# Kernel tuning notes

Hardware: AMD Instinct MI355X
Metric: run time of the kernel (lower is better)

Reference implementation:

```python
import jax, jax.numpy as jnp
import numpy as np

# ---- config ----
N = 500000
C = 32            # output_coordinate_dim
RES = [256, 256, 256, 64]
J = 2             # wavelet levels
BOUNDS = 1.3
# plane i -> (H, W) of stored plane, and (q, r) coord indices into [x,y,z,t]
# grid_sample convention: coord0 indexes W, coord1 indexes H
PLANE_RES = [(256, 256), (256, 256), (256, 64), (256, 256), (256, 64), (256, 64)]
COORD_IDX = [(0, 1), (0, 2), (3, 0), (1, 2), (3, 1), (3, 2)]

# coif4 decomposition low-pass filter (pywt), 24 taps
DEC_LO = np.array([
    -1.7849850030882614e-06, -3.2596802368833675e-06, 3.1229875865345646e-05,
    6.233903446100713e-05, -0.00025997455248771324, -0.0005890207562443383,
    0.0012665619292989445, 0.003751436157278457, -0.00565828668661072,
    -0.015211731527946259, 0.025082261844864097, 0.03933442712333749,
    -0.09622044203398798, -0.06662747426342504, 0.4343860564914685,
    0.782238930920499, 0.41530840703043026, -0.05607731331675481,
    -0.08126669968087875, 0.026682300156053072, 0.016068943964776348,
    -0.0073461663276420935, -0.0016294920126017326, 0.0008923136685823146],
    dtype=np.float32)
REC_LO = DEC_LO[::-1].copy()                                    # synthesis low-pass
REC_HI = (DEC_LO * ((-1.0) ** np.arange(DEC_LO.shape[0]))).astype(np.float32)  # QMF high-pass


def _up2(x, axis):
    """Insert zeros between samples along axis (upsample by 2)."""
    x = jnp.moveaxis(x, axis, -1)
    z = jnp.zeros(x.shape[:-1] + (2 * x.shape[-1],), x.dtype)
    z = z.at[..., ::2].set(x)
    return jnp.moveaxis(z, -1, axis)


def _circ_conv(x, f, axis):
    """Circular convolution along axis with a short fixed filter (periodization mode)."""
    out = f[0] * x
    for k in range(1, len(f)):
        out = out + f[k] * jnp.roll(x, k, axis=axis)
    return out


def _sfb1d(lo, hi, axis):
    """1D synthesis filter bank: upsample, filter, add. Length L -> 2L."""
    return _circ_conv(_up2(lo, axis), REC_LO, axis) + _circ_conv(_up2(hi, axis), REC_HI, axis)


def _sfb_level(ll, yh):
    """One inverse-DWT level. ll: [1,C,h,w], yh: [1,C,3,h,w] -> [1,C,2h,2w]."""
    lh, hl, hh = yh[:, :, 0], yh[:, :, 1], yh[:, :, 2]
    lo = _sfb1d(ll, lh, axis=2)   # combine along H
    hi = _sfb1d(hl, hh, axis=2)
    return _sfb1d(lo, hi, axis=3)  # combine along W


def _idwt2(yl, yhb, yha):
    """2-level inverse DWT (coif4, periodization). yl coarsest, yhb coarse detail, yha fine detail."""
    x = _sfb_level(yl, yhb)   # H/4 -> H/2
    x = _sfb_level(x, yha)    # H/2 -> H
    return x                  # [1, C, H, W]


def _bilinear_sample(plane, coords):
    """torch.grid_sample(bilinear, align_corners=True) equivalent.
    plane: [C,H,W]; coords: [N,2] in [-1,1], coords[:,0]->W, coords[:,1]->H. Returns [N,C]."""
    Cc, H, W = plane.shape
    x = jnp.clip((coords[:, 0] + 1.0) * 0.5 * (W - 1), 0.0, W - 1.0)
    y = jnp.clip((coords[:, 1] + 1.0) * 0.5 * (H - 1), 0.0, H - 1.0)
    x0 = jnp.clip(jnp.floor(x), 0.0, W - 2.0)
    y0 = jnp.clip(jnp.floor(y), 0.0, H - 2.0)
    wx = x - x0
    wy = y - y0
    x0i = x0.astype(jnp.int32); x1i = x0i + 1
    y0i = y0.astype(jnp.int32); y1i = y0i + 1
    v = (plane[:, y0i, x0i] * (1 - wy) * (1 - wx)
         + plane[:, y0i, x1i] * (1 - wy) * wx
         + plane[:, y1i, x0i] * wy * (1 - wx)
         + plane[:, y1i, x1i] * wy * wx)  # [C,N]
    return v.T


def setup_inputs() -> dict:
    key = jax.random.key(0)
    keys = jax.random.split(key, 2 + 6 * 3)
    inp = {}
    inp["pts"] = jax.random.uniform(keys[0], (N, 3), jnp.float32, -BOUNDS, BOUNDS)
    inp["timestamps"] = jax.random.uniform(keys[1], (N, 1), jnp.float32, 0.0, 1.0)
    for i, (H, W) in enumerate(PLANE_RES):
        k0, k1, k2 = keys[2 + 3 * i], keys[2 + 3 * i + 1], keys[2 + 3 * i + 2]
        # wavelet-domain learned parameters: yl coarsest approx, yha fine detail, yhb coarse detail
        inp[f"yl{i}"] = 0.3 + 0.1 * jax.random.normal(k0, (1, C, H // 4, W // 4), jnp.float32)
        inp[f"yha{i}"] = 0.05 * jax.random.normal(k1, (1, C, 3, H // 2, W // 2), jnp.float32)
        inp[f"yhb{i}"] = 0.05 * jax.random.normal(k2, (1, C, 3, H // 4, W // 4), jnp.float32)
    return inp


def reference(pts, timestamps,
              yl0, yha0, yhb0, yl1, yha1, yhb1, yl2, yha2, yhb2,
              yl3, yha3, yhb3, yl4, yha4, yhb4, yl5, yha5, yhb5):
    coefs = [(yl0, yha0, yhb0), (yl1, yha1, yhb1), (yl2, yha2, yhb2),
             (yl3, yha3, yhb3), (yl4, yha4, yhb4), (yl5, yha5, yhb5)]
    # normalize_aabb with aabb = [[B,B,B],[-B,-B,-B]]
    pts_n = (pts - BOUNDS) * (2.0 / (-2.0 * BOUNDS)) - 1.0
    t = timestamps * 2.0 - 1.0
    p4 = jnp.concatenate([pts_n, t], axis=-1)  # [N,4] = (x,y,z,t) in [-1,1]
    interp = jnp.ones((), jnp.float32)
    for (yl, yha, yhb), (q, r) in zip(coefs, COORD_IDX):
        plane = _idwt2(yl, yhb, yha)[0]                      # [C,H,W] IDWT reconstruction
        coords = jnp.stack([p4[:, q], p4[:, r]], axis=-1)    # [N,2]
        feat = _bilinear_sample(plane, coords)               # [N,C] gather
        interp = interp * feat                               # multiplicative fusion
    return interp
```

## Files before the change

### kernel.cpp

```cpp
#include <hip/hip_runtime.h>
#include <hip/hip_fp16.h>

#define NBIN 4096
#define CAP 256
#define OVCAP 65536

__device__ __constant__ float DEC_LO[24] = {
    -1.7849850030882614e-06f, -3.2596802368833675e-06f, 3.1229875865345646e-05f,
    6.233903446100713e-05f, -0.00025997455248771324f, -0.0005890207562443383f,
    0.0012665619292989445f, 0.003751436157278457f, -0.00565828668661072f,
    -0.015211731527946259f, 0.025082261844864097f, 0.03933442712333749f,
    -0.09622044203398798f, -0.06662747426342504f, 0.4343860564914685f,
    0.782238930920499f, 0.41530840703043026f, -0.05607731331675481f,
    -0.08126669968087875f, 0.026682300156053072f, 0.016068943964776348f,
    -0.0073461663276420935f, -0.0016294920126017326f, 0.0008923136685823146f
};

struct PK {
    const float* yl[6];
    const float* yhb[6];
    const float* yha[6];
    float* x1[6];
    __half* lo2[6];
    __half* hi2[6];
    __half* planeH[6];
    const float* pts;
    const float* ts;
    int* cnt;
    float4* binP4;
    int* binIdx;
    float4* ovP4;
    int* ovIdx;
    int Npts;
};

__device__ __forceinline__ void compute_p4(const float* pts, const float* ts, int p, float* p4) {
    const float sc = (float)(2.0 / (-2.0 * 1.3));
    p4[0] = (pts[p * 3 + 0] - 1.3f) * sc - 1.0f;
    p4[1] = (pts[p * 3 + 1] - 1.3f) * sc - 1.0f;
    p4[2] = (pts[p * 3 + 2] - 1.3f) * sc - 1.0f;
    p4[3] = ts[p] * 2.0f - 1.0f;
}

__device__ __forceinline__ int morton_key(const float* p4) {
    int key = 0;
#pragma unroll
    for (int d = 0; d < 4; ++d) {
        float u = (p4[d] + 1.0f) * 0.5f * 8.0f;
        int ci = (int)u;
        ci = ci < 0 ? 0 : (ci > 7 ? 7 : ci);
#pragma unroll
        for (int b = 0; b < 3; ++b) key |= ((ci >> b) & 1) << (b * 4 + d);
    }
    return key;
}

__global__ __launch_bounds__(256) void k1_l1_zero(PK a) {
    __shared__ struct { float lo[32 * 64], hi[32 * 64]; } sm;
    int bid = blockIdx.x, tid = threadIdx.x;

    if (bid < 768) {
        int rg = bid & 3, c = (bid >> 2) & 31, i = bid >> 7;
        int w4 = (i == 0 || i == 1 || i == 3) ? 64 : 16;
        int lw4 = (w4 == 64) ? 6 : 4;

        const float* llc = a.yl[i] + (size_t)c * 64 * w4;
        const float* lhc = a.yhb[i] + (size_t)(c * 3 + 0) * 64 * w4;
        const float* hlc = a.yhb[i] + (size_t)(c * 3 + 1) * 64 * w4;
        const float* hhc = a.yhb[i] + (size_t)(c * 3 + 2) * 64 * w4;

        for (int idx = tid; idx < (16 << lw4); idx += 256) {
            int mp = idx >> lw4, x = idx & (w4 - 1);
            int m = rg * 16 + mp;
            float lo0 = 0.f, lo1 = 0.f, hi0 = 0.f, hi1 = 0.f;
#pragma unroll
            for (int j = 0; j < 12; ++j) {
                int r = (m - j) & 63;
                int ii = (r << lw4) + x;
                float vll = llc[ii], vlh = lhc[ii], vhl = hlc[ii], vhh = hhc[ii];
                float rl0 = DEC_LO[23 - 2 * j], rl1 = DEC_LO[22 - 2 * j];
                float rh0 = DEC_LO[2 * j],      rh1 = -DEC_LO[2 * j + 1];
                lo0 += rl0 * vll + rh0 * vlh;
                lo1 += rl1 * vll + rh1 * vlh;
                hi0 += rl0 * vhl + rh0 * vhh;
                hi1 += rl1 * vhl + rh1 * vhh;
            }
            sm.lo[((2 * mp) << lw4) + x] = lo0;
            sm.lo[((2 * mp + 1) << lw4) + x] = lo1;
            sm.hi[((2 * mp) << lw4) + x] = hi0;
            sm.hi[((2 * mp + 1) << lw4) + x] = hi1;
        }
        __syncthreads();

        int w2 = w4 * 2;
        float* x1p = a.x1[i] + (size_t)c * 128 * w2;
        for (int idx = tid; idx < (32 << lw4); idx += 256) {
            int yl = idx >> lw4, mcol = idx & (w4 - 1);
            float o0 = 0.f, o1 = 0.f;
#pragma unroll
            for (int j = 0; j < 12; ++j) {
                int r = (mcol - j) & (w4 - 1);
                float vl = sm.lo[(yl << lw4) + r], vh = sm.hi[(yl << lw4) + r];
                o0 += DEC_LO[23 - 2 * j] * vl + DEC_LO[2 * j] * vh;
                o1 += DEC_LO[22 - 2 * j] * vl - DEC_LO[2 * j + 1] * vh;
            }
            *(float2*)(x1p + (size_t)(rg * 32 + yl) * w2 + 2 * mcol) = make_float2(o0, o1);
        }
    } else {
        int idx = (bid - 768) * 256 + tid;
        if (idx <= NBIN) a.cnt[idx] = 0;
    }
}

__global__ __launch_bounds__(256) void k2_v2_scatter(PK a) {
    int bid = blockIdx.x, tid = threadIdx.x;

    if (bid < 7680) {
        const int boff[7] = {0, 2048, 4096, 4608, 6656, 7168, 7680};
        int i = 0;
        while (i < 5 && bid >= boff[i + 1]) ++i;
        int lw2 = (i == 0 || i == 1 || i == 3) ? 7 : 5;
        int w2 = 1 << lw2;
        unsigned t = (unsigned)(bid - boff[i]) * 256u + tid;
        unsigned hw = 128u << lw2;
        unsigned c = t >> (7 + lw2);
        unsigned rem = t & (hw - 1);
        unsigned m = rem >> lw2;
        unsigned x = rem & (unsigned)(w2 - 1);

        const float* llc = a.x1[i] + (size_t)c * hw;
        const float* lhc = a.yha[i] + (size_t)(c * 3 + 0) * hw;
        const float* hlc = a.yha[i] + (size_t)(c * 3 + 1) * hw;
        const float* hhc = a.yha[i] + (size_t)(c * 3 + 2) * hw;

        float lo0 = 0.f, lo1 = 0.f, hi0 = 0.f, hi1 = 0.f;
#pragma unroll
        for (int j = 0; j < 12; ++j) {
            int r = ((int)m - j) & 127;
            unsigned idx = ((unsigned)r << lw2) + x;
            float vll = llc[idx], vlh = lhc[idx], vhl = hlc[idx], vhh = hhc[idx];
            float rl0 = DEC_LO[23 - 2 * j], rl1 = DEC_LO[22 - 2 * j];
            float rh0 = DEC_LO[2 * j],      rh1 = -DEC_LO[2 * j + 1];
            lo0 += rl0 * vll + rh0 * vlh;
            lo1 += rl1 * vll + rh1 * vlh;
            hi0 += rl0 * vhl + rh0 * vhh;
            hi1 += rl1 * vhl + rh1 * vhh;
        }
        size_t ob = ((size_t)c * 256 + 2 * m) * w2 + x;
        a.lo2[i][ob] = __float2half(lo0);
        a.lo2[i][ob + w2] = __float2half(lo1);
        a.hi2[i][ob] = __float2half(hi0);
        a.hi2[i][ob + w2] = __float2half(hi1);
    } else {
        for (int p = (bid - 7680) * 256 + tid; p < a.Npts; p += 512 * 256) {
            float p4[4];
            compute_p4(a.pts, a.ts, p, p4);
            int key = morton_key(p4);
            int pos = atomicAdd(&a.cnt[key], 1);
            if (pos < CAP) {
                a.binP4[key * CAP + pos] = make_float4(p4[0], p4[1], p4[2], p4[3]);
                a.binIdx[key * CAP + pos] = p;
            } else {
                int ov = atomicAdd(&a.cnt[NBIN], 1);
                if (ov < OVCAP) {
                    a.ovP4[ov] = make_float4(p4[0], p4[1], p4[2], p4[3]);
                    a.ovIdx[ov] = p;
                }
            }
        }
    }
}

__global__ __launch_bounds__(256) void k3_ht(PK a) {
    __shared__ struct { __half lo[32 * 130], hi[32 * 130]; } sm;
    int bid = blockIdx.x, tid = threadIdx.x;
    int i = bid >> 8, y = bid & 255;
    int lw2 = (i == 0 || i == 1 || i == 3) ? 7 : 5;
    int w2 = 1 << lw2;
    int stride = w2 + 2;

    for (int idx = tid; idx < (32 << lw2); idx += 256) {
        int c = idx >> lw2, x = idx & (w2 - 1);
        size_t g = ((size_t)c * 256 + y) * w2 + x;
        sm.lo[c * stride + x] = a.lo2[i][g];
        sm.hi[c * stride + x] = a.hi2[i][g];
    }
    __syncthreads();

    int W = 2 * w2;
    __half* orow = a.planeH[i] + (size_t)y * W * 32;
    for (int idx = tid; idx < (32 << lw2); idx += 256) {
        int m = idx >> 5, c = idx & 31;
        float o0 = 0.f, o1 = 0.f;
#pragma unroll
        for (int j = 0; j < 12; ++j) {
            int r2 = m - j; if (r2 < 0) r2 += w2;
            float vl = __half2float(sm.lo[c * stride + r2]);
            float vh = __half2float(sm.hi[c * stride + r2]);
            o0 += DEC_LO[23 - 2 * j] * vl + DEC_LO[2 * j] * vh;
            o1 += DEC_LO[22 - 2 * j] * vl - DEC_LO[2 * j + 1] * vh;
        }
        orow[(2 * m) * 32 + c] = __float2half(o0);
        orow[(2 * m + 1) * 32 + c] = __float2half(o1);
    }
}

union H8 { float4 f4; __half h[8]; };

struct SK {
    const __half* pl[6];
    const float4* binP4;
    const int* binIdx;
    const int* cnt;
    const float4* ovP4;
    const int* ovIdx;
    float* out;
};

__device__ __forceinline__ void sample_point(const SK& a, const float* p4, int oidx, int ch8) {
    const int PW[6] = {256, 256, 64, 256, 64, 64};
    const int QI[6] = {0, 0, 3, 1, 3, 3};
    const int RI[6] = {1, 2, 0, 2, 1, 2};
    float acc[8] = {1.f, 1.f, 1.f, 1.f, 1.f, 1.f, 1.f, 1.f};
#pragma unroll
    for (int i = 0; i < 6; ++i) {
        int W = PW[i];
        float cx = p4[QI[i]];
        float cy = p4[RI[i]];
        float fx = (cx + 1.0f) * 0.5f * (float)(W - 1);
        fx = fminf(fmaxf(fx, 0.0f), (float)(W - 1));
        float fy = (cy + 1.0f) * 0.5f * 255.0f;
        fy = fminf(fmaxf(fy, 0.0f), 255.0f);
        float x0 = fminf(fmaxf(floorf(fx), 0.0f), (float)(W - 2));
        float y0 = fminf(fmaxf(floorf(fy), 0.0f), 254.0f);
        float wx = fx - x0, wy = fy - y0;
        int xi = (int)x0, yi = (int)y0;

        const __half* base = a.pl[i] + ((size_t)yi * W + xi) * 32 + ch8;
        H8 u00, u01, u10, u11;
        u00.f4 = *(const float4*)(base);
        u01.f4 = *(const float4*)(base + 32);
        u10.f4 = *(const float4*)(base + (size_t)W * 32);
        u11.f4 = *(const float4*)(base + (size_t)W * 32 + 32);

        float w00 = (1.f - wy) * (1.f - wx), w01 = (1.f - wy) * wx;
        float w10 = wy * (1.f - wx), w11 = wy * wx;
#pragma unroll
        for (int k = 0; k < 8; ++k) {
            float f = w00 * __half2float(u00.h[k]) + w01 * __half2float(u01.h[k]) +
                      w10 * __half2float(u10.h[k]) + w11 * __half2float(u11.h[k]);
            acc[k] *= f;
        }
    }
    float* op = a.out + (size_t)oidx * 32 + ch8;
    *(float4*)(op) = make_float4(acc[0], acc[1], acc[2], acc[3]);
    *(float4*)(op + 4) = make_float4(acc[4], acc[5], acc[6], acc[7]);
}

__global__ __launch_bounds__(256) void k4_sample(SK a) {
    int bid = blockIdx.x, tid = threadIdx.x;
    if (bid < NBIN) {
        int bin = (bid & 7) * (NBIN / 8) + (bid >> 3);
        int n = a.cnt[bin];
        n = n < CAP ? n : CAP;
        const float4* bp = a.binP4 + bin * CAP;
        const int* bi = a.binIdx + bin * CAP;
        for (int l = tid; l < n * 4; l += 256) {
            int s = l >> 2, ch8 = (l & 3) << 3;
            float4 q = bp[s];
            float p4[4] = {q.x, q.y, q.z, q.w};
            sample_point(a, p4, bi[s], ch8);
        }
    } else {
        int ov = a.cnt[NBIN];
        ov = ov < OVCAP ? ov : OVCAP;
        for (int l = (bid - NBIN) * 256 + tid; l < ov * 4; l += 8 * 256) {
            int s = l >> 2, ch8 = (l & 3) << 3;
            float4 q = a.ovP4[s];
            float p4[4] = {q.x, q.y, q.z, q.w};
            sample_point(a, p4, a.ovIdx[s], ch8);
        }
    }
}

extern "C" void kernel_launch(void* const* d_in, const int* in_sizes, int n_in,
                              void* d_out, int out_size, void* d_ws, size_t ws_size,
                              hipStream_t stream) {
    const int PWt[6] = {256, 256, 64, 256, 64, 64};
    const int Npts = in_sizes[0] / 3;

    char* ws = (char*)d_ws;
    PK a;
    size_t off = 0;
    for (int i = 0; i < 6; ++i) {
        int W = PWt[i], w2 = W / 2;
        a.x1[i] = (float*)(ws + off);      off += (size_t)32 * 128 * w2 * 4;
        a.lo2[i] = (__half*)(ws + off);    off += (size_t)32 * 256 * w2 * 2;
        a.hi2[i] = (__half*)(ws + off);    off += (size_t)32 * 256 * w2 * 2;
        a.planeH[i] = (__half*)(ws + off); off += (size_t)256 * W * 32 * 2;
    }
    off = (off + 15) & ~(size_t)15;
    a.binP4 = (float4*)(ws + off);  off += (size_t)NBIN * CAP * 16;
    a.ovP4 = (float4*)(ws + off);   off += (size_t)OVCAP * 16;
    a.binIdx = (int*)(ws + off);    off += (size_t)NBIN * CAP * 4;
    a.ovIdx = (int*)(ws + off);     off += (size_t)OVCAP * 4;
    a.cnt = (int*)(ws + off);       off += (NBIN + 1) * 4;

    a.pts = (const float*)d_in[0];
    a.ts = (const float*)d_in[1];
    for (int i = 0; i < 6; ++i) {
        a.yl[i] = (const float*)d_in[2 + 3 * i];
        a.yha[i] = (const float*)d_in[3 + 3 * i];
        a.yhb[i] = (const float*)d_in[4 + 3 * i];
    }
    a.Npts = Npts;

    k1_l1_zero<<<768 + 17, 256, 0, stream>>>(a);
    k2_v2_scatter<<<7680 + 512, 256, 0, stream>>>(a);
    k3_ht<<<1536, 256, 0, stream>>>(a);

    SK s;
    for (int i = 0; i < 6; ++i) s.pl[i] = a.planeH[i];
    s.binP4 = a.binP4; s.binIdx = a.binIdx; s.cnt = a.cnt;
    s.ovP4 = a.ovP4; s.ovIdx = a.ovIdx;
    s.out = (float*)d_out;
    k4_sample<<<NBIN + 8, 256, 0, stream>>>(s);
}
```

Baseline: 274.3 us.

## Aggregate bin counts in shared memory, vectorize vertical filter, split sample bins

The scatter phase now runs on 32 blocks that build a per-block shared-memory histogram of Morton keys. Each block reserves its ranges with one global atomic per nonzero bin and then scatters points using shared atomics, which cuts global atomic contention. The vertical synthesis filter processes two columns per thread with float2 loads and half2 stores, halving its block count, and its blocks are interleaved. The sampling kernel splits each bin across two blocks. The tradeoffs are that only 32 blocks handle binning, each computing the point coordinates twice, and that points within a bin now follow a block-ordered layout.

```diff
diff --git a/kernel.cpp b/kernel.cpp
--- a/kernel.cpp
+++ b/kernel.cpp
@@ -4,6 +4,7 @@
 #define NBIN 4096
 #define CAP 256
 #define OVCAP 65536
+#define NSB 32
 
 __device__ __constant__ float DEC_LO[24] = {
     -1.7849850030882614e-06f, -3.2596802368833675e-06f, 3.1229875865345646e-05f,
@@ -113,50 +114,35 @@
 }
 
 __global__ __launch_bounds__(256) void k2_v2_scatter(PK a) {
+    __shared__ int hist[NBIN];
     int bid = blockIdx.x, tid = threadIdx.x;
 
-    if (bid < 7680) {
-        const int boff[7] = {0, 2048, 4096, 4608, 6656, 7168, 7680};
-        int i = 0;
-        while (i < 5 && bid >= boff[i + 1]) ++i;
-        int lw2 = (i == 0 || i == 1 || i == 3) ? 7 : 5;
-        int w2 = 1 << lw2;
-        unsigned t = (unsigned)(bid - boff[i]) * 256u + tid;
-        unsigned hw = 128u << lw2;
-        unsigned c = t >> (7 + lw2);
-        unsigned rem = t & (hw - 1);
-        unsigned m = rem >> lw2;
-        unsigned x = rem & (unsigned)(w2 - 1);
-
-        const float* llc = a.x1[i] + (size_t)c * hw;
-        const float* lhc = a.yha[i] + (size_t)(c * 3 + 0) * hw;
-        const float* hlc = a.yha[i] + (size_t)(c * 3 + 1) * hw;
-        const float* hhc = a.yha[i] + (size_t)(c * 3 + 2) * hw;
-
-        float lo0 = 0.f, lo1 = 0.f, hi0 = 0.f, hi1 = 0.f;
-#pragma unroll
-        for (int j = 0; j < 12; ++j) {
-            int r = ((int)m - j) & 127;
-            unsigned idx = ((unsigned)r << lw2) + x;
-            float vll = llc[idx], vlh = lhc[idx], vhl = hlc[idx], vhh = hhc[idx];
-            float rl0 = DEC_LO[23 - 2 * j], rl1 = DEC_LO[22 - 2 * j];
-            float rh0 = DEC_LO[2 * j],      rh1 = -DEC_LO[2 * j + 1];
-            lo0 += rl0 * vll + rh0 * vlh;
-            lo1 += rl1 * vll + rh1 * vlh;
-            hi0 += rl0 * vhl + rh0 * vhh;
-            hi1 += rl1 * vhl + rh1 * vhh;
-        }
-        size_t ob = ((size_t)c * 256 + 2 * m) * w2 + x;
-        a.lo2[i][ob] = __float2half(lo0);
-        a.lo2[i][ob + w2] = __float2half(lo1);
-        a.hi2[i][ob] = __float2half(hi0);
-        a.hi2[i][ob + w2] = __float2half(hi1);
-    } else {
-        for (int p = (bid - 7680) * 256 + tid; p < a.Npts; p += 512 * 256) {
+    if (bid < NSB) {
+        for (int b = tid; b < NBIN; b += 256) hist[b] = 0;
+        __syncthreads();
+
+        int chunk = (a.Npts + NSB - 1) / NSB;
+        int p0 = bid * chunk;
+        int p1 = p0 + chunk; if (p1 > a.Npts) p1 = a.Npts;
+
+        for (int p = p0 + tid; p < p1; p += 256) {
+            float p4[4];
+            compute_p4(a.pts, a.ts, p, p4);
+            atomicAdd(&hist[morton_key(p4)], 1);
+        }
+        __syncthreads();
+
+        for (int b = tid; b < NBIN; b += 256) {
+            int h = hist[b];
+            if (h > 0) hist[b] = atomicAdd(&a.cnt[b], h);
+        }
+        __syncthreads();
+
+        for (int p = p0 + tid; p < p1; p += 256) {
             float p4[4];
             compute_p4(a.pts, a.ts, p, p4);
             int key = morton_key(p4);
-            int pos = atomicAdd(&a.cnt[key], 1);
+            int pos = atomicAdd(&hist[key], 1);
             if (pos < CAP) {
                 a.binP4[key * CAP + pos] = make_float4(p4[0], p4[1], p4[2], p4[3]);
                 a.binIdx[key * CAP + pos] = p;
@@ -168,6 +154,50 @@
                 }
             }
         }
+    } else {
+        int ib = bid - NSB;
+        ib = (ib & 7) * 480 + (ib >> 3);
+
+        const int boff[7] = {0, 1024, 2048, 2304, 3328, 3584, 3840};
+        int i = 0;
+        while (i < 5 && ib >= boff[i + 1]) ++i;
+        int lw2 = (i == 0 || i == 1 || i == 3) ? 7 : 5;
+        int w2 = 1 << lw2;
+        unsigned t = (unsigned)(ib - boff[i]) * 256u + tid;
+        unsigned hp = 128u << (lw2 - 1);
+        unsigned c = t >> (6 + lw2);
+        unsigned rem = t & (hp - 1);
+        unsigned m = rem >> (lw2 - 1);
+        unsigned x = (rem & (unsigned)((w2 >> 1) - 1)) * 2;
+        unsigned hw = 128u << lw2;
+
+        const float* llc = a.x1[i] + (size_t)c * hw;
+        const float* lhc = a.yha[i] + (size_t)(c * 3 + 0) * hw;
+        const float* hlc = a.yha[i] + (size_t)(c * 3 + 1) * hw;
+        const float* hhc = a.yha[i] + (size_t)(c * 3 + 2) * hw;
+
+        float lo0a = 0.f, lo0b = 0.f, lo1a = 0.f, lo1b = 0.f;
+        float hi0a = 0.f, hi0b = 0.f, hi1a = 0.f, hi1b = 0.f;
+#pragma unroll
+        for (int j = 0; j < 12; ++j) {
+            int r = ((int)m - j) & 127;
+            unsigned idx = ((unsigned)r << lw2) + x;
+            float2 vll = *(const float2*)(llc + idx);
+            float2 vlh = *(const float2*)(lhc + idx);
+            float2 vhl = *(const float2*)(hlc + idx);
+            float2 vhh = *(const float2*)(hhc + idx);
+            float rl0 = DEC_LO[23 - 2 * j], rl1 = DEC_LO[22 - 2 * j];
+            float rh0 = DEC_LO[2 * j],      rh1 = -DEC_LO[2 * j + 1];
+            lo0a += rl0 * vll.x + rh0 * vlh.x;  lo0b += rl0 * vll.y + rh0 * vlh.y;
+            lo1a += rl1 * vll.x + rh1 * vlh.x;  lo1b += rl1 * vll.y + rh1 * vlh.y;
+            hi0a += rl0 * vhl.x + rh0 * vhh.x;  hi0b += rl0 * vhl.y + rh0 * vhh.y;
+            hi1a += rl1 * vhl.x + rh1 * vhh.x;  hi1b += rl1 * vhl.y + rh1 * vhh.y;
+        }
+        size_t ob = ((size_t)c * 256 + 2 * m) * w2 + x;
+        *(__half2*)(a.lo2[i] + ob)      = __floats2half2_rn(lo0a, lo0b);
+        *(__half2*)(a.lo2[i] + ob + w2) = __floats2half2_rn(lo1a, lo1b);
+        *(__half2*)(a.hi2[i] + ob)      = __floats2half2_rn(hi0a, hi0b);
+        *(__half2*)(a.hi2[i] + ob + w2) = __floats2half2_rn(hi1a, hi1b);
     }
 }
 
@@ -259,13 +289,15 @@
 
 __global__ __launch_bounds__(256) void k4_sample(SK a) {
     int bid = blockIdx.x, tid = threadIdx.x;
-    if (bid < NBIN) {
-        int bin = (bid & 7) * (NBIN / 8) + (bid >> 3);
+    if (bid < 2 * NBIN) {
+        int b = bid & (NBIN - 1);
+        int half = bid >> 12;
+        int bin = (b & 7) * (NBIN / 8) + (b >> 3);
         int n = a.cnt[bin];
         n = n < CAP ? n : CAP;
         const float4* bp = a.binP4 + bin * CAP;
         const int* bi = a.binIdx + bin * CAP;
-        for (int l = tid; l < n * 4; l += 256) {
+        for (int l = half * 256 + tid; l < n * 4; l += 512) {
             int s = l >> 2, ch8 = (l & 3) << 3;
             float4 q = bp[s];
             float p4[4] = {q.x, q.y, q.z, q.w};
@@ -274,7 +306,7 @@
     } else {
         int ov = a.cnt[NBIN];
         ov = ov < OVCAP ? ov : OVCAP;
-        for (int l = (bid - NBIN) * 256 + tid; l < ov * 4; l += 8 * 256) {
+        for (int l = (bid - 2 * NBIN) * 256 + tid; l < ov * 4; l += 8 * 256) {
             int s = l >> 2, ch8 = (l & 3) << 3;
             float4 q = a.ovP4[s];
             float p4[4] = {q.x, q.y, q.z, q.w};
@@ -316,7 +348,7 @@
     a.Npts = Npts;
 
     k1_l1_zero<<<768 + 17, 256, 0, stream>>>(a);
-    k2_v2_scatter<<<7680 + 512, 256, 0, stream>>>(a);
+    k2_v2_scatter<<<NSB + 3840, 256, 0, stream>>>(a);
     k3_ht<<<1536, 256, 0, stream>>>(a);
 
     SK s;
@@ -324,5 +356,5 @@
     s.binP4 = a.binP4; s.binIdx = a.binIdx; s.cnt = a.cnt;
     s.ovP4 = a.ovP4; s.ovIdx = a.ovIdx;
     s.out = (float*)d_out;
-    k4_sample<<<NBIN + 8, 256, 0, stream>>>(s);
-}
+    k4_sample<<<2 * NBIN + 8, 256, 0, stream>>>(s);
+}
```

Result: slower. 300.2 us (+9.4%).
